# Kernel tuning notes

Hardware: AMD Instinct MI355X
Metric: run time of the kernel (lower is better)

The kernel has to match this reference:

```python
import jax, jax.numpy as jnp
import numpy as np

N = 100000
E = 1600000
D_IN, D_HID, D_OUT = 256, 256, 40


def setup_inputs() -> dict:
    key = jax.random.key(0)
    ks = jax.random.split(key, 8)
    x = jax.random.normal(ks[0], (N, D_IN), dtype=jnp.float32)
    W1 = jax.random.normal(ks[1], (D_IN, D_HID), dtype=jnp.float32) * (1.0 / np.sqrt(D_IN))
    b1 = jnp.zeros((D_HID,), dtype=jnp.float32)
    W2 = jax.random.normal(ks[2], (D_HID, D_HID), dtype=jnp.float32) * (1.0 / np.sqrt(D_HID))
    b2 = jnp.zeros((D_HID,), dtype=jnp.float32)
    W3 = jax.random.normal(ks[3], (D_HID, D_OUT), dtype=jnp.float32) * (1.0 / np.sqrt(D_HID))
    b3 = jnp.zeros((D_OUT,), dtype=jnp.float32)
    src = jax.random.randint(ks[4], (E,), 0, N, dtype=jnp.int32)
    dst = jax.random.randint(ks[5], (E,), 0, N, dtype=jnp.int32)
    return {"x": x, "W1": W1, "b1": b1, "W2": W2, "b2": b2, "W3": W3, "b3": b3,
            "src": src, "dst": dst}


def _degrees(src, dst):
    ones = jnp.ones((src.shape[0],), dtype=jnp.float32)
    out_deg = jax.ops.segment_sum(ones, src, num_segments=N)
    in_deg = jax.ops.segment_sum(ones, dst, num_segments=N)
    # DGL norm='both': clamp to avoid div-by-zero for isolated nodes
    inv_sqrt_out = jnp.where(out_deg > 0, jax.lax.rsqrt(jnp.maximum(out_deg, 1.0)), 0.0)
    inv_sqrt_in = jnp.where(in_deg > 0, jax.lax.rsqrt(jnp.maximum(in_deg, 1.0)), 0.0)
    return inv_sqrt_out, inv_sqrt_in


def _graph_conv(x, W, b, src, dst, inv_sqrt_out, inv_sqrt_in):
    # h = D_in^{-1/2} A (D_out^{-1/2} x) W + b   (symmetric-normalized SpMM)
    h = x * inv_sqrt_out[:, None]
    agg = jax.ops.segment_sum(h[src], dst, num_segments=N)  # [N, D]
    agg = agg * inv_sqrt_in[:, None]
    return agg @ W + b


def reference(x, W1, b1, W2, b2, W3, b3, src, dst):
    inv_sqrt_out, inv_sqrt_in = _degrees(src, dst)
    h = jax.nn.relu(_graph_conv(x, W1, b1, src, dst, inv_sqrt_out, inv_sqrt_in))
    # dropout is identity at inference (training=False)
    h = jax.nn.relu(_graph_conv(h, W2, b2, src, dst, inv_sqrt_out, inv_sqrt_in))
    h = _graph_conv(h, W3, b3, src, dst, inv_sqrt_out, inv_sqrt_in)
    return jax.nn.log_softmax(h, axis=-1)
```

## Files before the change

### kernel.cpp

```cpp
#include <hip/hip_runtime.h>
#include <hip/hip_bf16.h>
#include <math.h>

#define D 256
#define DOUT 40

typedef __attribute__((ext_vector_type(8))) short short8;
typedef __attribute__((ext_vector_type(4))) float f32x4;

__device__ __forceinline__ float lo_bf(unsigned w) {
    union { unsigned u; float f; } c; c.u = w << 16; return c.f;
}
__device__ __forceinline__ float hi_bf(unsigned w) {
    union { unsigned u; float f; } c; c.u = w & 0xffff0000u; return c.f;
}
__device__ __forceinline__ float b2f(unsigned short u) {
    union { unsigned u; float f; } c; c.u = ((unsigned)u) << 16; return c.f;
}
__device__ __forceinline__ unsigned short f2b(float f) {
    __hip_bfloat16 h = __float2bfloat16(f);
    return reinterpret_cast<unsigned short&>(h);
}

__global__ __launch_bounds__(256) void k_degree(const int* __restrict__ src,
                                                const int* __restrict__ dst,
                                                int* __restrict__ outdeg,
                                                int* __restrict__ indeg, int E) {
    int e = blockIdx.x * 256 + threadIdx.x;
    if (e < E) {
        atomicAdd(&outdeg[src[e]], 1);
        atomicAdd(&indeg[dst[e]], 1);
    }
}

__global__ __launch_bounds__(256) void k_invsqrt(const int* __restrict__ outdeg,
                                                 const int* __restrict__ indeg,
                                                 float* __restrict__ inv_out,
                                                 float* __restrict__ inv_in, int n) {
    int i = blockIdx.x * 256 + threadIdx.x;
    if (i < n) {
        int od = outdeg[i], idg = indeg[i];
        inv_out[i] = od > 0 ? rsqrtf((float)od) : 0.0f;
        inv_in[i]  = idg > 0 ? rsqrtf((float)idg) : 0.0f;
    }
}

__global__ __launch_bounds__(1024) void k_scan1(const int* __restrict__ deg,
                                                int* __restrict__ offs,
                                                int* __restrict__ bsum, int n) {
    __shared__ int wsum[16];
    int tid = threadIdx.x, lane = tid & 63, wv = tid >> 6;
    int i = blockIdx.x * 1024 + tid;
    int v = (i < n) ? deg[i] : 0;
    int x = v;
    #pragma unroll
    for (int o = 1; o < 64; o <<= 1) {
        int t = __shfl_up(x, o);
        if (lane >= o) x += t;
    }
    if (lane == 63) wsum[wv] = x;
    __syncthreads();
    if (wv == 0 && lane < 16) {
        int y = wsum[lane];
        #pragma unroll
        for (int o = 1; o < 16; o <<= 1) {
            int t = __shfl_up(y, o);
            if (lane >= o) y += t;
        }
        wsum[lane] = y;
    }
    __syncthreads();
    int waveoff = wv ? wsum[wv - 1] : 0;
    if (i < n) offs[i] = waveoff + x - v;
    if (tid == 0) bsum[blockIdx.x] = wsum[15];
}

__global__ __launch_bounds__(64) void k_scan2(int* __restrict__ bsum, int G) {
    int lane = threadIdx.x;
    int carry = 0;
    for (int base = 0; base < G; base += 64) {
        int idx = base + lane;
        int v = (idx < G) ? bsum[idx] : 0;
        int x = v;
        #pragma unroll
        for (int o = 1; o < 64; o <<= 1) {
            int t = __shfl_up(x, o);
            if (lane >= o) x += t;
        }
        int tot = __shfl(x, 63);
        if (idx < G) bsum[idx] = carry + x - v;
        carry += tot;
    }
}

__global__ __launch_bounds__(1024) void k_scan3(int* __restrict__ offs,
                                                const int* __restrict__ bsum,
                                                int n, int E) {
    int i = blockIdx.x * 1024 + threadIdx.x;
    if (i < n) offs[i] += bsum[blockIdx.x];
    if (i == 0) offs[n] = E;
}

__global__ __launch_bounds__(256) void k_scatter(const int* __restrict__ src,
                                                 const int* __restrict__ dst,
                                                 const int* __restrict__ offs,
                                                 int* __restrict__ cursor,
                                                 const float* __restrict__ inv_out,
                                                 int* __restrict__ csr_src,
                                                 float* __restrict__ csr_w, int E) {
    int e = blockIdx.x * 256 + threadIdx.x;
    if (e < E) {
        int d = dst[e], s = src[e];
        int p = atomicAdd(&cursor[d], 1);
        int idx = offs[d] + p;
        csr_src[idx] = s;
        csr_w[idx] = inv_out[s];
    }
}

__global__ __launch_bounds__(256) void k_cvt_x(const float* __restrict__ in,
                                               unsigned short* __restrict__ out,
                                               long long n8) {
    long long i = (long long)blockIdx.x * 256 + threadIdx.x;
    if (i >= n8) return;
    const float4* p = reinterpret_cast<const float4*>(in) + i * 2;
    float4 a = p[0], b = p[1];
    uint4 o;
    o.x = (unsigned)f2b(a.x) | ((unsigned)f2b(a.y) << 16);
    o.y = (unsigned)f2b(a.z) | ((unsigned)f2b(a.w) << 16);
    o.z = (unsigned)f2b(b.x) | ((unsigned)f2b(b.y) << 16);
    o.w = (unsigned)f2b(b.z) | ((unsigned)f2b(b.w) << 16);
    reinterpret_cast<uint4*>(out)[i] = o;
}

__global__ __launch_bounds__(256) void k_cvt_wt(const float* __restrict__ W,
                                                unsigned short* __restrict__ Wt) {
    int n = blockIdx.x, k = threadIdx.x;
    Wt[n * 256 + k] = f2b(W[k * 256 + n]);
}

__global__ __launch_bounds__(256) void k_cvt_wt3(const float* __restrict__ W3,
                                                 unsigned short* __restrict__ Wt3) {
    int n = blockIdx.x, k = threadIdx.x;
    float v = (n < DOUT) ? W3[k * DOUT + n] : 0.0f;
    Wt3[n * 256 + k] = f2b(v);
}

__global__ __launch_bounds__(256) void k_spmm256b(const unsigned short* __restrict__ h,
                                                  const int* __restrict__ offs,
                                                  const int* __restrict__ csr_src,
                                                  const float* __restrict__ csr_w,
                                                  const float* __restrict__ inv_in,
                                                  unsigned short* __restrict__ out, int n) {
    int wid = (blockIdx.x * 256 + threadIdx.x) >> 6;
    int lane = threadIdx.x & 63;
    if (wid >= n) return;
    int beg = offs[wid], end = offs[wid + 1];
    float a0 = 0.f, a1 = 0.f, a2 = 0.f, a3 = 0.f;
    int j = beg;
    for (; j + 4 <= end; j += 4) {
        int s0 = csr_src[j], s1 = csr_src[j + 1], s2 = csr_src[j + 2], s3 = csr_src[j + 3];
        float w0 = csr_w[j], w1 = csr_w[j + 1], w2 = csr_w[j + 2], w3 = csr_w[j + 3];
        uint2 v0 = reinterpret_cast<const uint2*>(h + (size_t)s0 * D)[lane];
        uint2 v1 = reinterpret_cast<const uint2*>(h + (size_t)s1 * D)[lane];
        uint2 v2 = reinterpret_cast<const uint2*>(h + (size_t)s2 * D)[lane];
        uint2 v3 = reinterpret_cast<const uint2*>(h + (size_t)s3 * D)[lane];
        a0 += w0 * lo_bf(v0.x); a1 += w0 * hi_bf(v0.x); a2 += w0 * lo_bf(v0.y); a3 += w0 * hi_bf(v0.y);
        a0 += w1 * lo_bf(v1.x); a1 += w1 * hi_bf(v1.x); a2 += w1 * lo_bf(v1.y); a3 += w1 * hi_bf(v1.y);
        a0 += w2 * lo_bf(v2.x); a1 += w2 * hi_bf(v2.x); a2 += w2 * lo_bf(v2.y); a3 += w2 * hi_bf(v2.y);
        a0 += w3 * lo_bf(v3.x); a1 += w3 * hi_bf(v3.x); a2 += w3 * lo_bf(v3.y); a3 += w3 * hi_bf(v3.y);
    }
    for (; j < end; ++j) {
        int s = csr_src[j];
        float w = csr_w[j];
        uint2 v = reinterpret_cast<const uint2*>(h + (size_t)s * D)[lane];
        a0 += w * lo_bf(v.x); a1 += w * hi_bf(v.x); a2 += w * lo_bf(v.y); a3 += w * hi_bf(v.y);
    }
    float sc = inv_in[wid];
    uint2 r;
    r.x = (unsigned)f2b(sc * a0) | ((unsigned)f2b(sc * a1) << 16);
    r.y = (unsigned)f2b(sc * a2) | ((unsigned)f2b(sc * a3) << 16);
    reinterpret_cast<uint2*>(out + (size_t)wid * D)[lane] = r;
}

__global__ __launch_bounds__(256) void k_gemm_mfma(const unsigned short* __restrict__ A,
                                                   const unsigned short* __restrict__ Wt,
                                                   const float* __restrict__ bias,
                                                   unsigned short* __restrict__ C,
                                                   int M, int ldc, int ncols, int flags) {
    __shared__ unsigned short As[128][40];
    __shared__ unsigned short Bs[128][40];
    int tid = threadIdx.x;
    int lane = tid & 63, wave = tid >> 6;
    int wr = wave >> 1, wc = wave & 1;
    int rowBase = blockIdx.x * 128;
    int colBase = blockIdx.y * 128;

    f32x4 acc[4][4];
    #pragma unroll
    for (int m = 0; m < 4; ++m)
        #pragma unroll
        for (int n = 0; n < 4; ++n) acc[m][n] = (f32x4){0.f, 0.f, 0.f, 0.f};

    int ar = lane & 15, kg = lane >> 4;

    for (int k0 = 0; k0 < 256; k0 += 32) {
        #pragma unroll
        for (int hh = 0; hh < 2; ++hh) {
            int c = tid + hh * 256;
            int row = c >> 2, kc = c & 3;
            int grow = rowBase + row;
            uint4 v = make_uint4(0, 0, 0, 0);
            if (grow < M)
                v = *reinterpret_cast<const uint4*>(A + (size_t)grow * 256 + k0 + kc * 8);
            *reinterpret_cast<uint4*>(&As[row][kc * 8]) = v;
        }
        #pragma unroll
        for (int hh = 0; hh < 2; ++hh) {
            int c = tid + hh * 256;
            int col = c >> 2, kc = c & 3;
            int gcol = colBase + col;
            uint4 v = *reinterpret_cast<const uint4*>(Wt + (size_t)gcol * 256 + k0 + kc * 8);
            *reinterpret_cast<uint4*>(&Bs[col][kc * 8]) = v;
        }
        __syncthreads();
        short8 a[4], b[4];
        #pragma unroll
        for (int m = 0; m < 4; ++m)
            a[m] = *reinterpret_cast<const short8*>(&As[wr * 64 + m * 16 + ar][kg * 8]);
        #pragma unroll
        for (int n = 0; n < 4; ++n)
            b[n] = *reinterpret_cast<const short8*>(&Bs[wc * 64 + n * 16 + ar][kg * 8]);
        #pragma unroll
        for (int m = 0; m < 4; ++m)
            #pragma unroll
            for (int n = 0; n < 4; ++n)
                acc[m][n] = __builtin_amdgcn_mfma_f32_16x16x32_bf16(a[m], b[n], acc[m][n], 0, 0, 0);
        __syncthreads();
    }

    int rq = lane >> 4, cl = lane & 15;
    float bv[4];
    #pragma unroll
    for (int n = 0; n < 4; ++n) {
        int col = colBase + wc * 64 + n * 16 + cl;
        bv[n] = ((flags & 2) && col < ncols) ? bias[col] : 0.f;
    }
    #pragma unroll
    for (int m = 0; m < 4; ++m) {
        #pragma unroll
        for (int n = 0; n < 4; ++n) {
            int col = colBase + wc * 64 + n * 16 + cl;
            if (col >= ncols) continue;
            #pragma unroll
            for (int r = 0; r < 4; ++r) {
                int row = rowBase + wr * 64 + m * 16 + rq * 4 + r;
                if (row < M) {
                    float v = acc[m][n][r] + bv[n];
                    if (flags & 1) v = fmaxf(v, 0.f);
                    C[(size_t)row * ldc + col] = f2b(v);
                }
            }
        }
    }
}

__global__ __launch_bounds__(256) void k_gemm_mfma64(const unsigned short* __restrict__ A,
                                                     const unsigned short* __restrict__ Wt,
                                                     unsigned short* __restrict__ C,
                                                     int M, int ldc, int ncols) {
    __shared__ unsigned short As[128][40];
    __shared__ unsigned short Bs[64][40];
    int tid = threadIdx.x;
    int lane = tid & 63, wave = tid >> 6;
    int rowBase = blockIdx.x * 128;

    f32x4 acc[2][4];
    #pragma unroll
    for (int m = 0; m < 2; ++m)
        #pragma unroll
        for (int n = 0; n < 4; ++n) acc[m][n] = (f32x4){0.f, 0.f, 0.f, 0.f};

    int ar = lane & 15, kg = lane >> 4;

    for (int k0 = 0; k0 < 256; k0 += 32) {
        #pragma unroll
        for (int hh = 0; hh < 2; ++hh) {
            int c = tid + hh * 256;
            int row = c >> 2, kc = c & 3;
            int grow = rowBase + row;
            uint4 v = make_uint4(0, 0, 0, 0);
            if (grow < M)
                v = *reinterpret_cast<const uint4*>(A + (size_t)grow * 256 + k0 + kc * 8);
            *reinterpret_cast<uint4*>(&As[row][kc * 8]) = v;
        }
        {
            int col = tid >> 2, kc = tid & 3;
            uint4 v = *reinterpret_cast<const uint4*>(Wt + (size_t)col * 256 + k0 + kc * 8);
            *reinterpret_cast<uint4*>(&Bs[col][kc * 8]) = v;
        }
        __syncthreads();
        short8 a[2], b[4];
        #pragma unroll
        for (int m = 0; m < 2; ++m)
            a[m] = *reinterpret_cast<const short8*>(&As[wave * 32 + m * 16 + ar][kg * 8]);
        #pragma unroll
        for (int n = 0; n < 4; ++n)
            b[n] = *reinterpret_cast<const short8*>(&Bs[n * 16 + ar][kg * 8]);
        #pragma unroll
        for (int m = 0; m < 2; ++m)
            #pragma unroll
            for (int n = 0; n < 4; ++n)
                acc[m][n] = __builtin_amdgcn_mfma_f32_16x16x32_bf16(a[m], b[n], acc[m][n], 0, 0, 0);
        __syncthreads();
    }

    int rq = lane >> 4, cl = lane & 15;
    #pragma unroll
    for (int m = 0; m < 2; ++m) {
        #pragma unroll
        for (int n = 0; n < 4; ++n) {
            int col = n * 16 + cl;
            if (col >= ncols) continue;
            #pragma unroll
            for (int r = 0; r < 4; ++r) {
                int row = rowBase + wave * 32 + m * 16 + rq * 4 + r;
                if (row < M) C[(size_t)row * ldc + col] = f2b(acc[m][n][r]);
            }
        }
    }
}

__global__ __launch_bounds__(256) void k_spmm40_lsm(const unsigned short* __restrict__ y,
                                                    const int* __restrict__ offs,
                                                    const int* __restrict__ csr_src,
                                                    const float* __restrict__ csr_w,
                                                    const float* __restrict__ inv_in,
                                                    const float* __restrict__ b3,
                                                    float* __restrict__ out, int n) {
    int wid = (blockIdx.x * 256 + threadIdx.x) >> 6;
    int lane = threadIdx.x & 63;
    if (wid >= n) return;
    int beg = offs[wid], end = offs[wid + 1];
    float acc = 0.f;
    int j = beg;
    for (; j + 4 <= end; j += 4) {
        int s0 = csr_src[j], s1 = csr_src[j + 1], s2 = csr_src[j + 2], s3 = csr_src[j + 3];
        float w0 = csr_w[j], w1 = csr_w[j + 1], w2 = csr_w[j + 2], w3 = csr_w[j + 3];
        float v0 = b2f(y[(size_t)s0 * DOUT + lane]);
        float v1 = b2f(y[(size_t)s1 * DOUT + lane]);
        float v2 = b2f(y[(size_t)s2 * DOUT + lane]);
        float v3 = b2f(y[(size_t)s3 * DOUT + lane]);
        acc += w0 * v0 + w1 * v1 + w2 * v2 + w3 * v3;
    }
    for (; j < end; ++j) {
        int s = csr_src[j];
        acc += csr_w[j] * b2f(y[(size_t)s * DOUT + lane]);
    }
    bool act = lane < DOUT;
    float v = act ? fmaf(inv_in[wid], acc, b3[lane]) : -INFINITY;
    float m = v;
    #pragma unroll
    for (int o = 32; o > 0; o >>= 1) m = fmaxf(m, __shfl_xor(m, o));
    float e = act ? __expf(v - m) : 0.f;
    float ssum = e;
    #pragma unroll
    for (int o = 32; o > 0; o >>= 1) ssum += __shfl_xor(ssum, o);
    float ls = logf(ssum);
    if (act) out[(size_t)wid * DOUT + lane] = v - m - ls;
}

extern "C" void kernel_launch(void* const* d_in, const int* in_sizes, int n_in,
                              void* d_out, int out_size, void* d_ws, size_t ws_size,
                              hipStream_t stream) {
    const float* x  = (const float*)d_in[0];
    const float* W1 = (const float*)d_in[1];
    const float* b1 = (const float*)d_in[2];
    const float* W2 = (const float*)d_in[3];
    const float* b2 = (const float*)d_in[4];
    const float* W3 = (const float*)d_in[5];
    const float* b3 = (const float*)d_in[6];
    const int* src  = (const int*)d_in[7];
    const int* dst  = (const int*)d_in[8];
    const int N = in_sizes[0] / D;
    const int E = in_sizes[7];
    float* out = (float*)d_out;

    char* p = (char*)d_ws;
    auto alloc = [&](size_t bytes) {
        char* r = p;
        p += (bytes + 255) & ~(size_t)255;
        return r;
    };
    int*   zeroz   = (int*)alloc((size_t)3 * N * sizeof(int));
    int*   offs    = (int*)alloc((size_t)(N + 1) * sizeof(int));
    int*   bsum    = (int*)alloc((size_t)1024 * sizeof(int));
    int*   csr_src = (int*)alloc((size_t)E * sizeof(int));
    float* inv_out = (float*)alloc((size_t)N * sizeof(float));
    float* inv_in  = (float*)alloc((size_t)N * sizeof(float));
    float* csr_w   = (float*)alloc((size_t)E * sizeof(float));
    unsigned short* Wt1 = (unsigned short*)alloc((size_t)256 * 256 * 2);
    unsigned short* Wt2 = (unsigned short*)alloc((size_t)256 * 256 * 2);
    unsigned short* Wt3 = (unsigned short*)alloc((size_t)64 * 256 * 2);
    unsigned short* buf0 = (unsigned short*)alloc((size_t)N * D * 2);
    unsigned short* buf1 = (unsigned short*)alloc((size_t)N * D * 2);
    unsigned short* buf2 = (unsigned short*)alloc((size_t)N * D * 2);
    int* outdeg = zeroz;
    int* indeg  = zeroz + N;
    int* cursor = zeroz + 2 * N;

    hipMemsetAsync(zeroz, 0, (size_t)3 * N * sizeof(int), stream);
    k_degree<<<(E + 255) / 256, 256, 0, stream>>>(src, dst, outdeg, indeg, E);
    k_invsqrt<<<(N + 255) / 256, 256, 0, stream>>>(outdeg, indeg, inv_out, inv_in, N);
    int G = (N + 1023) / 1024;
    k_scan1<<<G, 1024, 0, stream>>>(indeg, offs, bsum, N);
    k_scan2<<<1, 64, 0, stream>>>(bsum, G);
    k_scan3<<<G, 1024, 0, stream>>>(offs, bsum, N, E);
    k_scatter<<<(E + 255) / 256, 256, 0, stream>>>(src, dst, offs, cursor, inv_out,
                                                   csr_src, csr_w, E);

    k_cvt_wt<<<256, 256, 0, stream>>>(W1, Wt1);
    k_cvt_wt<<<256, 256, 0, stream>>>(W2, Wt2);
    k_cvt_wt3<<<64, 256, 0, stream>>>(W3, Wt3);

    long long n8 = (long long)N * D / 8;
    k_cvt_x<<<(int)((n8 + 255) / 256), 256, 0, stream>>>(x, buf0, n8);

    dim3 gemmGrid((N + 127) / 128, 2);
    k_spmm256b<<<(N + 3) / 4, 256, 0, stream>>>(buf0, offs, csr_src, csr_w, inv_in, buf1, N);
    k_gemm_mfma<<<gemmGrid, 256, 0, stream>>>(buf1, Wt1, b1, buf2, N, 256, 256, 3);
    k_spmm256b<<<(N + 3) / 4, 256, 0, stream>>>(buf2, offs, csr_src, csr_w, inv_in, buf0, N);
    k_gemm_mfma<<<gemmGrid, 256, 0, stream>>>(buf0, Wt2, b2, buf1, N, 256, 256, 3);
    k_gemm_mfma64<<<(N + 127) / 128, 256, 0, stream>>>(buf1, Wt3, buf0, N, DOUT, DOUT);
    k_spmm40_lsm<<<(N + 3) / 4, 256, 0, stream>>>(buf0, offs, csr_src, csr_w, inv_in,
                                                  b3, out, N);
}
```

Measured before the change: 813.3 us.

## Privatize degree histograms, fuse layer-2 and layer-3 GEMMs, unroll SpMM gather by 8

Degree counting and CSR scatter now use 32 per-block private histograms with workgroup-scope atomics, followed by a column reduction that produces degrees, an exclusive per-block cursor and the inverse square roots. This removes the memset and the global contended atomics. The layer-2 GEMM (with bias and ReLU) and the layer-3 projection are fused into one kernel that keeps the hidden tile in LDS, so the intermediate 256-wide activation is never written to or read from global memory. The SpMM inner loop is unrolled to 8 gathers in flight for more memory-level parallelism. In exchange, the histogram stage uses only 32 blocks and large scratch arrays, and the fused kernel needs a lot of LDS, which may limit occupancy.

```diff
diff --git a/kernel.cpp b/kernel.cpp
--- a/kernel.cpp
+++ b/kernel.cpp
@@ -4,6 +4,7 @@
 
 #define D 256
 #define DOUT 40
+#define HB 32
 
 typedef __attribute__((ext_vector_type(8))) short short8;
 typedef __attribute__((ext_vector_type(4))) float f32x4;
@@ -22,27 +23,45 @@
     return reinterpret_cast<unsigned short&>(h);
 }
 
-__global__ __launch_bounds__(256) void k_degree(const int* __restrict__ src,
-                                                const int* __restrict__ dst,
-                                                int* __restrict__ outdeg,
-                                                int* __restrict__ indeg, int E) {
-    int e = blockIdx.x * 256 + threadIdx.x;
-    if (e < E) {
-        atomicAdd(&outdeg[src[e]], 1);
-        atomicAdd(&indeg[dst[e]], 1);
-    }
-}
-
-__global__ __launch_bounds__(256) void k_invsqrt(const int* __restrict__ outdeg,
-                                                 const int* __restrict__ indeg,
-                                                 float* __restrict__ inv_out,
-                                                 float* __restrict__ inv_in, int n) {
+__global__ __launch_bounds__(1024) void k_hist(const int* __restrict__ src,
+                                               const int* __restrict__ dst,
+                                               unsigned* __restrict__ inH,
+                                               unsigned* __restrict__ outH,
+                                               int n, int E) {
+    unsigned* myIn  = inH  + (size_t)blockIdx.x * n;
+    unsigned* myOut = outH + (size_t)blockIdx.x * n;
+    for (int i = threadIdx.x; i < n; i += 1024) { myIn[i] = 0u; myOut[i] = 0u; }
+    __syncthreads();
+    int per = (E + HB - 1) / HB;
+    int lo = blockIdx.x * per;
+    int hi = min(E, lo + per);
+    for (int e = lo + threadIdx.x; e < hi; e += 1024) {
+        int d = __builtin_nontemporal_load(dst + e);
+        int s = __builtin_nontemporal_load(src + e);
+        __hip_atomic_fetch_add(&myIn[d], 1u, __ATOMIC_RELAXED, __HIP_MEMORY_SCOPE_WORKGROUP);
+        __hip_atomic_fetch_add(&myOut[s], 1u, __ATOMIC_RELAXED, __HIP_MEMORY_SCOPE_WORKGROUP);
+    }
+}
+
+__global__ __launch_bounds__(256) void k_colred(unsigned* __restrict__ inH,
+                                                const unsigned* __restrict__ outH,
+                                                int* __restrict__ indeg,
+                                                float* __restrict__ inv_in,
+                                                float* __restrict__ inv_out, int n) {
     int i = blockIdx.x * 256 + threadIdx.x;
-    if (i < n) {
-        int od = outdeg[i], idg = indeg[i];
-        inv_out[i] = od > 0 ? rsqrtf((float)od) : 0.0f;
-        inv_in[i]  = idg > 0 ? rsqrtf((float)idg) : 0.0f;
-    }
+    if (i >= n) return;
+    unsigned accI = 0, accO = 0;
+    #pragma unroll 4
+    for (int b = 0; b < HB; ++b) {
+        size_t idx = (size_t)b * n + i;
+        unsigned t = inH[idx];
+        inH[idx] = accI;
+        accI += t;
+        accO += outH[idx];
+    }
+    indeg[i] = (int)accI;
+    inv_in[i]  = accI ? rsqrtf((float)accI) : 0.f;
+    inv_out[i] = accO ? rsqrtf((float)accO) : 0.f;
 }
 
 __global__ __launch_bounds__(1024) void k_scan1(const int* __restrict__ deg,
@@ -101,20 +120,26 @@
     if (i == 0) offs[n] = E;
 }
 
-__global__ __launch_bounds__(256) void k_scatter(const int* __restrict__ src,
-                                                 const int* __restrict__ dst,
-                                                 const int* __restrict__ offs,
-                                                 int* __restrict__ cursor,
-                                                 const float* __restrict__ inv_out,
-                                                 int* __restrict__ csr_src,
-                                                 float* __restrict__ csr_w, int E) {
-    int e = blockIdx.x * 256 + threadIdx.x;
-    if (e < E) {
-        int d = dst[e], s = src[e];
-        int p = atomicAdd(&cursor[d], 1);
-        int idx = offs[d] + p;
-        csr_src[idx] = s;
-        csr_w[idx] = inv_out[s];
+__global__ __launch_bounds__(1024) void k_scatter2(const int* __restrict__ src,
+                                                   const int* __restrict__ dst,
+                                                   const int* __restrict__ offs,
+                                                   unsigned* __restrict__ inH,
+                                                   const float* __restrict__ inv_out,
+                                                   int* __restrict__ csr_src,
+                                                   float* __restrict__ csr_w,
+                                                   int n, int E) {
+    unsigned* myCur = inH + (size_t)blockIdx.x * n;
+    int per = (E + HB - 1) / HB;
+    int lo = blockIdx.x * per;
+    int hi = min(E, lo + per);
+    for (int e = lo + threadIdx.x; e < hi; e += 1024) {
+        int d = __builtin_nontemporal_load(dst + e);
+        int s = __builtin_nontemporal_load(src + e);
+        unsigned r = __hip_atomic_fetch_add(&myCur[d], 1u, __ATOMIC_RELAXED,
+                                            __HIP_MEMORY_SCOPE_WORKGROUP);
+        int idx = offs[d] + (int)r;
+        __builtin_nontemporal_store(s, &csr_src[idx]);
+        __builtin_nontemporal_store(inv_out[s], &csr_w[idx]);
     }
 }
 
@@ -158,17 +183,18 @@
     int beg = offs[wid], end = offs[wid + 1];
     float a0 = 0.f, a1 = 0.f, a2 = 0.f, a3 = 0.f;
     int j = beg;
-    for (; j + 4 <= end; j += 4) {
-        int s0 = csr_src[j], s1 = csr_src[j + 1], s2 = csr_src[j + 2], s3 = csr_src[j + 3];
-        float w0 = csr_w[j], w1 = csr_w[j + 1], w2 = csr_w[j + 2], w3 = csr_w[j + 3];
-        uint2 v0 = reinterpret_cast<const uint2*>(h + (size_t)s0 * D)[lane];
-        uint2 v1 = reinterpret_cast<const uint2*>(h + (size_t)s1 * D)[lane];
-        uint2 v2 = reinterpret_cast<const uint2*>(h + (size_t)s2 * D)[lane];
-        uint2 v3 = reinterpret_cast<const uint2*>(h + (size_t)s3 * D)[lane];
-        a0 += w0 * lo_bf(v0.x); a1 += w0 * hi_bf(v0.x); a2 += w0 * lo_bf(v0.y); a3 += w0 * hi_bf(v0.y);
-        a0 += w1 * lo_bf(v1.x); a1 += w1 * hi_bf(v1.x); a2 += w1 * lo_bf(v1.y); a3 += w1 * hi_bf(v1.y);
-        a0 += w2 * lo_bf(v2.x); a1 += w2 * hi_bf(v2.x); a2 += w2 * lo_bf(v2.y); a3 += w2 * hi_bf(v2.y);
-        a0 += w3 * lo_bf(v3.x); a1 += w3 * hi_bf(v3.x); a2 += w3 * lo_bf(v3.y); a3 += w3 * hi_bf(v3.y);
+    for (; j + 8 <= end; j += 8) {
+        int s[8]; float w[8]; uint2 v[8];
+        #pragma unroll
+        for (int q = 0; q < 8; ++q) { s[q] = csr_src[j + q]; w[q] = csr_w[j + q]; }
+        #pragma unroll
+        for (int q = 0; q < 8; ++q)
+            v[q] = reinterpret_cast<const uint2*>(h + (size_t)s[q] * D)[lane];
+        #pragma unroll
+        for (int q = 0; q < 8; ++q) {
+            a0 += w[q] * lo_bf(v[q].x); a1 += w[q] * hi_bf(v[q].x);
+            a2 += w[q] * lo_bf(v[q].y); a3 += w[q] * hi_bf(v[q].y);
+        }
     }
     for (; j < end; ++j) {
         int s = csr_src[j];
@@ -186,8 +212,7 @@
 __global__ __launch_bounds__(256) void k_gemm_mfma(const unsigned short* __restrict__ A,
                                                    const unsigned short* __restrict__ Wt,
                                                    const float* __restrict__ bias,
-                                                   unsigned short* __restrict__ C,
-                                                   int M, int ldc, int ncols, int flags) {
+                                                   unsigned short* __restrict__ C, int M) {
     __shared__ unsigned short As[128][40];
     __shared__ unsigned short Bs[128][40];
     int tid = threadIdx.x;
@@ -219,8 +244,7 @@
         for (int hh = 0; hh < 2; ++hh) {
             int c = tid + hh * 256;
             int col = c >> 2, kc = c & 3;
-            int gcol = colBase + col;
-            uint4 v = *reinterpret_cast<const uint4*>(Wt + (size_t)gcol * 256 + k0 + kc * 8);
+            uint4 v = *reinterpret_cast<const uint4*>(Wt + (size_t)(colBase + col) * 256 + k0 + kc * 8);
             *reinterpret_cast<uint4*>(&Bs[col][kc * 8]) = v;
         }
         __syncthreads();
@@ -242,73 +266,75 @@
     int rq = lane >> 4, cl = lane & 15;
     float bv[4];
     #pragma unroll
-    for (int n = 0; n < 4; ++n) {
-        int col = colBase + wc * 64 + n * 16 + cl;
-        bv[n] = ((flags & 2) && col < ncols) ? bias[col] : 0.f;
-    }
+    for (int n = 0; n < 4; ++n) bv[n] = bias[colBase + wc * 64 + n * 16 + cl];
     #pragma unroll
     for (int m = 0; m < 4; ++m) {
         #pragma unroll
         for (int n = 0; n < 4; ++n) {
             int col = colBase + wc * 64 + n * 16 + cl;
-            if (col >= ncols) continue;
             #pragma unroll
             for (int r = 0; r < 4; ++r) {
                 int row = rowBase + wr * 64 + m * 16 + rq * 4 + r;
-                if (row < M) {
-                    float v = acc[m][n][r] + bv[n];
-                    if (flags & 1) v = fmaxf(v, 0.f);
-                    C[(size_t)row * ldc + col] = f2b(v);
-                }
+                if (row < M)
+                    C[(size_t)row * 256 + col] = f2b(fmaxf(acc[m][n][r] + bv[n], 0.f));
             }
         }
     }
 }
 
-__global__ __launch_bounds__(256) void k_gemm_mfma64(const unsigned short* __restrict__ A,
-                                                     const unsigned short* __restrict__ Wt,
-                                                     unsigned short* __restrict__ C,
-                                                     int M, int ldc, int ncols) {
+__global__ __launch_bounds__(512) void k_gemm_fuse23(const unsigned short* __restrict__ A,
+                                                     const unsigned short* __restrict__ Wt2,
+                                                     const float* __restrict__ b2,
+                                                     const unsigned short* __restrict__ Wt3,
+                                                     unsigned short* __restrict__ Z, int M) {
     __shared__ unsigned short As[128][40];
-    __shared__ unsigned short Bs[64][40];
+    __shared__ unsigned short Bs[256][40];
+    __shared__ unsigned short hS[128][264];
+    __shared__ unsigned short W3s[64][264];
     int tid = threadIdx.x;
     int lane = tid & 63, wave = tid >> 6;
+    int wr = wave >> 2, wc = wave & 3;
     int rowBase = blockIdx.x * 128;
-
-    f32x4 acc[2][4];
-    #pragma unroll
-    for (int m = 0; m < 2; ++m)
+    int ar = lane & 15, kg = lane >> 4;
+
+    for (int c = tid; c < 2048; c += 512) {
+        int row = c >> 5, kc = c & 31;
+        *reinterpret_cast<uint4*>(&W3s[row][kc * 8]) =
+            *reinterpret_cast<const uint4*>(Wt3 + (size_t)row * 256 + kc * 8);
+    }
+
+    f32x4 acc[4][4];
+    #pragma unroll
+    for (int m = 0; m < 4; ++m)
         #pragma unroll
         for (int n = 0; n < 4; ++n) acc[m][n] = (f32x4){0.f, 0.f, 0.f, 0.f};
 
-    int ar = lane & 15, kg = lane >> 4;
-
     for (int k0 = 0; k0 < 256; k0 += 32) {
-        #pragma unroll
-        for (int hh = 0; hh < 2; ++hh) {
-            int c = tid + hh * 256;
-            int row = c >> 2, kc = c & 3;
+        {
+            int row = tid >> 2, kc = tid & 3;
             int grow = rowBase + row;
             uint4 v = make_uint4(0, 0, 0, 0);
             if (grow < M)
                 v = *reinterpret_cast<const uint4*>(A + (size_t)grow * 256 + k0 + kc * 8);
             *reinterpret_cast<uint4*>(&As[row][kc * 8]) = v;
         }
-        {
-            int col = tid >> 2, kc = tid & 3;
-            uint4 v = *reinterpret_cast<const uint4*>(Wt + (size_t)col * 256 + k0 + kc * 8);
+        #pragma unroll
+        for (int hh = 0; hh < 2; ++hh) {
+            int c = tid + hh * 512;
+            int col = c >> 2, kc = c & 3;
+            uint4 v = *reinterpret_cast<const uint4*>(Wt2 + (size_t)col * 256 + k0 + kc * 8);
             *reinterpret_cast<uint4*>(&Bs[col][kc * 8]) = v;
         }
         __syncthreads();
-        short8 a[2], b[4];
-        #pragma unroll
-        for (int m = 0; m < 2; ++m)
-            a[m] = *reinterpret_cast<const short8*>(&As[wave * 32 + m * 16 + ar][kg * 8]);
+        short8 a[4], b[4];
+        #pragma unroll
+        for (int m = 0; m < 4; ++m)
+            a[m] = *reinterpret_cast<const short8*>(&As[wr * 64 + m * 16 + ar][kg * 8]);
         #pragma unroll
         for (int n = 0; n < 4; ++n)
-            b[n] = *reinterpret_cast<const short8*>(&Bs[n * 16 + ar][kg * 8]);
-        #pragma unroll
-        for (int m = 0; m < 2; ++m)
+            b[n] = *reinterpret_cast<const short8*>(&Bs[wc * 64 + n * 16 + ar][kg * 8]);
+        #pragma unroll
+        for (int m = 0; m < 4; ++m)
             #pragma unroll
             for (int n = 0; n < 4; ++n)
                 acc[m][n] = __builtin_amdgcn_mfma_f32_16x16x32_bf16(a[m], b[n], acc[m][n], 0, 0, 0);
@@ -317,16 +343,36 @@
 
     int rq = lane >> 4, cl = lane & 15;
     #pragma unroll
-    for (int m = 0; m < 2; ++m) {
-        #pragma unroll
-        for (int n = 0; n < 4; ++n) {
-            int col = n * 16 + cl;
-            if (col >= ncols) continue;
+    for (int n = 0; n < 4; ++n) {
+        int col = wc * 64 + n * 16 + cl;
+        float bb = b2[col];
+        #pragma unroll
+        for (int m = 0; m < 4; ++m)
             #pragma unroll
-            for (int r = 0; r < 4; ++r) {
-                int row = rowBase + wave * 32 + m * 16 + rq * 4 + r;
-                if (row < M) C[(size_t)row * ldc + col] = f2b(acc[m][n][r]);
-            }
+            for (int r = 0; r < 4; ++r)
+                hS[wr * 64 + m * 16 + rq * 4 + r][col] = f2b(fmaxf(acc[m][n][r] + bb, 0.f));
+    }
+    __syncthreads();
+
+    f32x4 acc2[3];
+    #pragma unroll
+    for (int n = 0; n < 3; ++n) acc2[n] = (f32x4){0.f, 0.f, 0.f, 0.f};
+    for (int k0 = 0; k0 < 256; k0 += 32) {
+        short8 a = *reinterpret_cast<const short8*>(&hS[wave * 16 + ar][k0 + kg * 8]);
+        #pragma unroll
+        for (int n = 0; n < 3; ++n) {
+            short8 b = *reinterpret_cast<const short8*>(&W3s[n * 16 + ar][k0 + kg * 8]);
+            acc2[n] = __builtin_amdgcn_mfma_f32_16x16x32_bf16(a, b, acc2[n], 0, 0, 0);
+        }
+    }
+    #pragma unroll
+    for (int n = 0; n < 3; ++n) {
+        int col = n * 16 + cl;
+        if (col >= DOUT) continue;
+        #pragma unroll
+        for (int r = 0; r < 4; ++r) {
+            int row = rowBase + wave * 16 + rq * 4 + r;
+            if (row < M) Z[(size_t)row * DOUT + col] = f2b(acc2[n][r]);
         }
     }
 }
@@ -392,7 +438,9 @@
         p += (bytes + 255) & ~(size_t)255;
         return r;
     };
-    int*   zeroz   = (int*)alloc((size_t)3 * N * sizeof(int));
+    unsigned* inH  = (unsigned*)alloc((size_t)HB * N * sizeof(unsigned));
+    unsigned* outH = (unsigned*)alloc((size_t)HB * N * sizeof(unsigned));
+    int*   indeg   = (int*)alloc((size_t)N * sizeof(int));
     int*   offs    = (int*)alloc((size_t)(N + 1) * sizeof(int));
     int*   bsum    = (int*)alloc((size_t)1024 * sizeof(int));
     int*   csr_src = (int*)alloc((size_t)E * sizeof(int));
@@ -405,19 +453,14 @@
     unsigned short* buf0 = (unsigned short*)alloc((size_t)N * D * 2);
     unsigned short* buf1 = (unsigned short*)alloc((size_t)N * D * 2);
     unsigned short* buf2 = (unsigned short*)alloc((size_t)N * D * 2);
-    int* outdeg = zeroz;
-    int* indeg  = zeroz + N;
-    int* cursor = zeroz + 2 * N;
-
-    hipMemsetAsync(zeroz, 0, (size_t)3 * N * sizeof(int), stream);
-    k_degree<<<(E + 255) / 256, 256, 0, stream>>>(src, dst, outdeg, indeg, E);
-    k_invsqrt<<<(N + 255) / 256, 256, 0, stream>>>(outdeg, indeg, inv_out, inv_in, N);
+
+    k_hist<<<HB, 1024, 0, stream>>>(src, dst, inH, outH, N, E);
+    k_colred<<<(N + 255) / 256, 256, 0, stream>>>(inH, outH, indeg, inv_in, inv_out, N);
     int G = (N + 1023) / 1024;
     k_scan1<<<G, 1024, 0, stream>>>(indeg, offs, bsum, N);
     k_scan2<<<1, 64, 0, stream>>>(bsum, G);
     k_scan3<<<G, 1024, 0, stream>>>(offs, bsum, N, E);
-    k_scatter<<<(E + 255) / 256, 256, 0, stream>>>(src, dst, offs, cursor, inv_out,
-                                                   csr_src, csr_w, E);
+    k_scatter2<<<HB, 1024, 0, stream>>>(src, dst, offs, inH, inv_out, csr_src, csr_w, N, E);
 
     k_cvt_wt<<<256, 256, 0, stream>>>(W1, Wt1);
     k_cvt_wt<<<256, 256, 0, stream>>>(W2, Wt2);
@@ -428,10 +471,9 @@
 
     dim3 gemmGrid((N + 127) / 128, 2);
     k_spmm256b<<<(N + 3) / 4, 256, 0, stream>>>(buf0, offs, csr_src, csr_w, inv_in, buf1, N);
-    k_gemm_mfma<<<gemmGrid, 256, 0, stream>>>(buf1, Wt1, b1, buf2, N, 256, 256, 3);
+    k_gemm_mfma<<<gemmGrid, 256, 0, stream>>>(buf1, Wt1, b1, buf2, N);
     k_spmm256b<<<(N + 3) / 4, 256, 0, stream>>>(buf2, offs, csr_src, csr_w, inv_in, buf0, N);
-    k_gemm_mfma<<<gemmGrid, 256, 0, stream>>>(buf0, Wt2, b2, buf1, N, 256, 256, 3);
-    k_gemm_mfma64<<<(N + 127) / 128, 256, 0, stream>>>(buf1, Wt3, buf0, N, DOUT, DOUT);
-    k_spmm40_lsm<<<(N + 3) / 4, 256, 0, stream>>>(buf0, offs, csr_src, csr_w, inv_in,
+    k_gemm_fuse23<<<(N + 127) / 128, 512, 0, stream>>>(buf0, Wt2, b2, Wt3, buf1, N);
+    k_spmm40_lsm<<<(N + 3) / 4, 256, 0, stream>>>(buf1, offs, csr_src, csr_w, inv_in,
                                                   b3, out, N);
 }
```

Measured after the change: 1.214 ms. 49.2% more time.
